# Optimization experiments

Hardware: AMD Instinct MI355X
Metric: run time of the kernel (lower is better)

The kernel has to match this reference:

```python
import jax, jax.numpy as jnp
import numpy as np

BATCH = 131072
INPUT_DIM = 256
HIDDEN = 128
DIM = 16
TRIL = DIM * (DIM + 1) // 2  # 136


def setup_inputs() -> dict:
    key = jax.random.key(0)
    k_x, k_w1, k_w2 = jax.random.split(key, 3)
    x = jax.random.normal(k_x, (BATCH, INPUT_DIM), dtype=jnp.float32)
    # Kaiming-ish init scaling so activations are well-conditioned
    W1 = jax.random.normal(k_w1, (INPUT_DIM, HIDDEN), dtype=jnp.float32) * (1.0 / np.sqrt(INPUT_DIM))
    b1 = jnp.zeros((HIDDEN,), dtype=jnp.float32)
    W2 = jax.random.normal(k_w2, (HIDDEN, TRIL), dtype=jnp.float32) * (1.0 / np.sqrt(HIDDEN))
    b2 = jnp.zeros((TRIL,), dtype=jnp.float32)
    return {"x": x, "W1": W1, "b1": b1, "W2": W2, "b2": b2}


def reference(x, W1, b1, W2, b2):
    # MLP: Linear -> ReLU -> Linear, producing tril entries of Cholesky factor
    h = jax.nn.relu(x @ W1 + b1)              # [B, 128]
    v = h @ W2 + b2                           # [B, 136]
    ti, tj = jnp.tril_indices(DIM)            # row-major tril order, matches torch.tril_indices
    L = jnp.zeros((x.shape[0], DIM, DIM), dtype=v.dtype).at[:, ti, tj].set(v)  # [B, D, D]
    rho = jnp.einsum('bik,bjk->bij', L, L)    # L @ L^T (real, so conj is no-op)
    trace = jnp.einsum('bii->b', rho)         # diagonal sum
    return rho / trace[:, None, None]
```

## Files before the change

### kernel.cpp

```cpp
#include <hip/hip_runtime.h>


typedef _Float16 h8 __attribute__((ext_vector_type(8)));
typedef float    f4 __attribute__((ext_vector_type(4)));
typedef int      i2 __attribute__((ext_vector_type(2)));

#define BATCH_N 131072
#define IN_DIM  256
#define HID     128
#define TRILN   136
#define BM      128
#define NT1     8
#define KS1     8
#define NT2     9
#define KS2     4
#define HSTR    136
#define LVSTR   160
#define PW1_N   (KS1*NT1*64*8)
#define PW2_N   (KS2*NT2*64*8)

__device__ __forceinline__ int rowoff(int i) {
    int g = i >> 2;
    return 4 * (g + 1) * (2 * g + (i & 3));
}

__global__ void pack_weights(const float* __restrict__ W1,
                             const float* __restrict__ W2,
                             _Float16* __restrict__ pw1,
                             _Float16* __restrict__ pw2) {
    int gid = blockIdx.x * blockDim.x + threadIdx.x;
    if (gid < PW1_N) {
        int j = gid & 7, l = (gid >> 3) & 63, f = gid >> 9;
        int ks = f >> 3, nt = f & 7;
        int k = ks * 32 + (l >> 4) * 8 + j;
        int n = nt * 16 + (l & 15);
        pw1[gid] = (_Float16)W1[k * HID + n];
    } else if (gid < PW1_N + PW2_N) {
        int g = gid - PW1_N;
        int j = g & 7, l = (g >> 3) & 63, f = g >> 9;
        int ks = f / NT2, nt = f - ks * NT2;
        int k = ks * 32 + (l >> 4) * 8 + j;
        int col = nt * 16 + (l & 15);
        pw2[g] = (col < TRILN) ? (_Float16)W2[k * TRILN + col] : (_Float16)0.0f;
    }
}

__device__ __forceinline__ h8 cvt_h8(f4 lo, f4 hi) {
    h8 r;
    r[0] = (_Float16)lo[0]; r[1] = (_Float16)lo[1];
    r[2] = (_Float16)lo[2]; r[3] = (_Float16)lo[3];
    r[4] = (_Float16)hi[0]; r[5] = (_Float16)hi[1];
    r[6] = (_Float16)hi[2]; r[7] = (_Float16)hi[3];
    return r;
}

__global__ __launch_bounds__(256, 4) void fused_mlp(
        const float* __restrict__ x, const float* __restrict__ b1,
        const float* __restrict__ b2, const _Float16* __restrict__ pw1,
        const _Float16* __restrict__ pw2, float* __restrict__ out) {
    __shared__ char smem_raw[BM * LVSTR * 2] __attribute__((aligned(16)));
    _Float16* hbuf = (_Float16*)smem_raw;
    _Float16* lv   = (_Float16*)smem_raw;

    const int tid  = threadIdx.x;
    const int w    = tid >> 6;
    const int lane = tid & 63;
    const int q    = lane >> 4;
    const int lm   = lane & 15;
    const int b0   = blockIdx.x * BM;

    f4 acc1[2][NT1];
    #pragma unroll
    for (int mt = 0; mt < 2; ++mt)
        #pragma unroll
        for (int nt = 0; nt < NT1; ++nt)
            acc1[mt][nt] = (f4){0.f, 0.f, 0.f, 0.f};

    const float* xr0 = x + (size_t)(b0 + w * 16 + lm) * IN_DIM + q * 8;
    const float* xr1 = xr0 + (size_t)64 * IN_DIM;

    f4 a0l = *(const f4*)xr0, a0h = *(const f4*)(xr0 + 4);
    f4 a1l = *(const f4*)xr1, a1h = *(const f4*)(xr1 + 4);

    #pragma unroll
    for (int ks = 0; ks < KS1; ++ks) {
        h8 bf[NT1];
        #pragma unroll
        for (int nt = 0; nt < NT1; ++nt)
            bf[nt] = *(const h8*)(pw1 + ((ks * NT1 + nt) * 64 + lane) * 8);
        h8 af0 = cvt_h8(a0l, a0h);
        h8 af1 = cvt_h8(a1l, a1h);
        if (ks + 1 < KS1) {
            const float* p0 = xr0 + (ks + 1) * 32;
            const float* p1 = xr1 + (ks + 1) * 32;
            a0l = *(const f4*)p0; a0h = *(const f4*)(p0 + 4);
            a1l = *(const f4*)p1; a1h = *(const f4*)(p1 + 4);
        }
        #pragma unroll
        for (int nt = 0; nt < NT1; ++nt) {
            acc1[0][nt] = __builtin_amdgcn_mfma_f32_16x16x32_f16(af0, bf[nt], acc1[0][nt], 0, 0, 0);
            acc1[1][nt] = __builtin_amdgcn_mfma_f32_16x16x32_f16(af1, bf[nt], acc1[1][nt], 0, 0, 0);
        }
    }

    {
        float b1v[NT1];
        #pragma unroll
        for (int nt = 0; nt < NT1; ++nt) b1v[nt] = b1[nt * 16 + lm];
        #pragma unroll
        for (int mt = 0; mt < 2; ++mt)
            #pragma unroll
            for (int nt = 0; nt < NT1; ++nt)
                #pragma unroll
                for (int r = 0; r < 4; ++r) {
                    float hv = acc1[mt][nt][r] + b1v[nt];
                    hv = fmaxf(hv, 0.f);
                    hbuf[(mt * 64 + w * 16 + q * 4 + r) * HSTR + nt * 16 + lm] = (_Float16)hv;
                }
    }

    f4 acc2[2][NT2];
    #pragma unroll
    for (int mt = 0; mt < 2; ++mt)
        #pragma unroll
        for (int nt = 0; nt < NT2; ++nt)
            acc2[mt][nt] = (f4){0.f, 0.f, 0.f, 0.f};

    #pragma unroll
    for (int ks = 0; ks < KS2; ++ks) {
        h8 ha0 = *(const h8*)(hbuf + (w * 16 + lm) * HSTR + ks * 32 + q * 8);
        h8 ha1 = *(const h8*)(hbuf + (64 + w * 16 + lm) * HSTR + ks * 32 + q * 8);
        #pragma unroll
        for (int nt = 0; nt < NT2; ++nt) {
            h8 bf = *(const h8*)(pw2 + ((ks * NT2 + nt) * 64 + lane) * 8);
            acc2[0][nt] = __builtin_amdgcn_mfma_f32_16x16x32_f16(ha0, bf, acc2[0][nt], 0, 0, 0);
            acc2[1][nt] = __builtin_amdgcn_mfma_f32_16x16x32_f16(ha1, bf, acc2[1][nt], 0, 0, 0);
        }
    }

    float b2v[NT2];
    #pragma unroll
    for (int nt = 0; nt < NT2; ++nt) {
        int col = nt * 16 + lm;
        b2v[nt] = (col < TRILN) ? b2[col] : 0.f;
    }

    float ps[2][4];
    #pragma unroll
    for (int mt = 0; mt < 2; ++mt)
        #pragma unroll
        for (int r = 0; r < 4; ++r) ps[mt][r] = 0.f;
    #pragma unroll
    for (int mt = 0; mt < 2; ++mt)
        #pragma unroll
        for (int nt = 0; nt < NT2; ++nt)
            #pragma unroll
            for (int r = 0; r < 4; ++r) {
                float v = acc2[mt][nt][r] + b2v[nt];
                ps[mt][r] += v * v;
            }

    float rinv[2][4];
    #pragma unroll
    for (int mt = 0; mt < 2; ++mt)
        #pragma unroll
        for (int r = 0; r < 4; ++r) {
            float s = ps[mt][r];
            s += __shfl_xor(s, 1);
            s += __shfl_xor(s, 2);
            s += __shfl_xor(s, 4);
            s += __shfl_xor(s, 8);
            rinv[mt][r] = 1.0f / s;
        }

    int voff[NT2];
    bool vok[NT2];
    #pragma unroll
    for (int nt = 0; nt < NT2; ++nt) {
        int c = nt * 16 + lm;
        vok[nt] = (c < TRILN);
        int cc = vok[nt] ? c : 0;
        int i = (int)((sqrtf(8.0f * (float)cc + 1.0f) - 1.0f) * 0.5f);
        int k = cc - (i * (i + 1)) / 2;
        voff[nt] = rowoff(i) + k;
    }

    __syncthreads();

    #pragma unroll
    for (int mt = 0; mt < 2; ++mt)
        #pragma unroll
        for (int r = 0; r < 4; ++r) {
            int base = (mt * 64 + w * 16 + q * 4 + r) * LVSTR;
            #pragma unroll
            for (int nt = 0; nt < NT2; ++nt)
                if (vok[nt])
                    lv[base + voff[nt]] = (_Float16)(acc2[mt][nt][r] + b2v[nt]);
        }

    int msk[4];
    {
        int n = lm - q * 8 + 1;
        #pragma unroll
        for (int p = 0; p < 4; ++p) {
            int c2 = n - 2 * p; c2 = c2 < 0 ? 0 : (c2 > 2 ? 2 : c2);
            msk[p] = (c2 == 2) ? ~0 : ((c2 == 1) ? 0xFFFF : 0);
        }
    }
    const int ro_lm = rowoff(lm);
    const f4 zero = (f4){0.f, 0.f, 0.f, 0.f};
    const int outcol = q * 64 + lm;

    #pragma unroll
    for (int mt = 0; mt < 2; ++mt)
        #pragma unroll
        for (int tq = 0; tq < 4; ++tq)
            #pragma unroll
            for (int r4 = 0; r4 < 4; ++r4) {
                int t = tq * 4 + r4;
                int row = mt * 64 + w * 16 + t;
                const _Float16* rp = lv + row * LVSTR + ro_lm + q * 8;
                i2 lo = *(const i2*)rp;
                i2 hi = *(const i2*)(rp + 4);
                h8 frag;
                ((i2*)&frag)[0] = (i2){lo.x & msk[0], lo.y & msk[1]};
                ((i2*)&frag)[1] = (i2){hi.x & msk[2], hi.y & msk[3]};
                f4 d = __builtin_amdgcn_mfma_f32_16x16x32_f16(frag, frag, zero, 0, 0, 0);
                float riv = __uint_as_float(
                    __builtin_amdgcn_readlane(__float_as_uint(rinv[mt][r4]), tq * 16));
                float* op = out + (size_t)(b0 + row) * 256 + outcol;
                #pragma unroll
                for (int sr = 0; sr < 4; ++sr)
                    op[sr * 16] = d[sr] * riv;
            }
}

extern "C" void kernel_launch(void* const* d_in, const int* in_sizes, int n_in,
                              void* d_out, int out_size, void* d_ws, size_t ws_size,
                              hipStream_t stream) {
    const float* x  = (const float*)d_in[0];
    const float* W1 = (const float*)d_in[1];
    const float* b1 = (const float*)d_in[2];
    const float* W2 = (const float*)d_in[3];
    const float* b2 = (const float*)d_in[4];
    float* out = (float*)d_out;

    _Float16* pw1 = (_Float16*)d_ws;
    _Float16* pw2 = pw1 + PW1_N;

    pack_weights<<<(PW1_N + PW2_N + 255) / 256, 256, 0, stream>>>(W1, W2, pw1, pw2);
    fused_mlp<<<BATCH_N / BM, 256, 0, stream>>>(x, b1, b2, pw1, pw2, out);
}
```

Before: 263.3 us.

## Process M-tiles sequentially per wave with private LDS regions and deeper x prefetch

Restructures the fused kernel so each wave handles its two 16-row M-tiles one after another instead of together. Each wave gets a private LDS region, so the block-wide __syncthreads is removed. The x loads for the second tile are prefetched during the first tile's epilogue, and the x prefetch depth goes from one k-step to four. This halves accumulator register pressure and lets memory loads overlap with compute, at the cost of less reuse of the W1/W2 fragments loaded per MFMA and twice the weight loads.

```diff
diff --git a/kernel.cpp b/kernel.cpp
--- a/kernel.cpp
+++ b/kernel.cpp
@@ -16,6 +16,7 @@
 #define KS2     4
 #define HSTR    136
 #define LVSTR   160
+#define MTREG   2560
 #define PW1_N   (KS1*NT1*64*8)
 #define PW2_N   (KS2*NT2*64*8)
 
@@ -54,13 +55,105 @@
     return r;
 }
 
+#define TAIL(MTBASE, MT)                                                       \
+  do {                                                                         \
+          \
+    _Pragma("unroll")                                                          \
+    for (int nt = 0; nt < NT1; ++nt) {                                         \
+      float b1v = b1[nt * 16 + lm];                                            \
+      _Pragma("unroll")                                                        \
+      for (int r = 0; r < 4; ++r) {                                            \
+        float hv = fmaxf(acc[nt][r] + b1v, 0.f);                               \
+        (MTBASE)[(q * 4 + r) * HSTR + nt * 16 + lm] = (_Float16)hv;            \
+      }                                                                        \
+    }                                                                          \
+                                                        \
+    f4 acc2[NT2];                                                              \
+    _Pragma("unroll")                                                          \
+    for (int nt = 0; nt < NT2; ++nt) acc2[nt] = (f4){0.f, 0.f, 0.f, 0.f};      \
+    _Pragma("unroll")                                                          \
+    for (int ks = 0; ks < KS2; ++ks) {                                         \
+      h8 ha = *(const h8*)((MTBASE) + lm * HSTR + ks * 32 + q * 8);            \
+      _Pragma("unroll")                                                        \
+      for (int nt = 0; nt < NT2; ++nt) {                                       \
+        h8 bf2 = *(const h8*)(pw2 + ((ks * NT2 + nt) * 64 + lane) * 8);        \
+        acc2[nt] = __builtin_amdgcn_mfma_f32_16x16x32_f16(ha, bf2, acc2[nt], 0, 0, 0); \
+      }                                                                        \
+    }                                                                          \
+    if ((MT) == 0) {                                                           \
+       \
+       \
+      _Pragma("unroll")                                                        \
+      for (int k = 0; k < 4; ++k) {                                            \
+        xp[2 * k]     = *(const f4*)(xr1 + k * 32);                            \
+        xp[2 * k + 1] = *(const f4*)(xr1 + k * 32 + 4);                        \
+      }                                                                        \
+      __builtin_amdgcn_sched_barrier(0);                                       \
+    }                                                                          \
+                                            \
+    float b2v[NT2];                                                            \
+    int voff[NT2]; bool vok[NT2];                                              \
+    _Pragma("unroll")                                                          \
+    for (int nt = 0; nt < NT2; ++nt) {                                         \
+      int c = nt * 16 + lm;                                                    \
+      vok[nt] = (c < TRILN);                                                   \
+      int cc = vok[nt] ? c : 0;                                                \
+      int i = (int)((sqrtf(8.0f * (float)cc + 1.0f) - 1.0f) * 0.5f);           \
+      int k = cc - (i * (i + 1)) / 2;                                          \
+      voff[nt] = rowoff(i) + k;                                                \
+      b2v[nt] = vok[nt] ? b2[c] : 0.f;                                         \
+    }                                                                          \
+       \
+    float rinv[4];                                                             \
+    _Pragma("unroll")                                                          \
+    for (int r = 0; r < 4; ++r) {                                              \
+      float s = 0.f;                                                           \
+      _Pragma("unroll")                                                        \
+      for (int nt = 0; nt < NT2; ++nt) {                                       \
+        float v = acc2[nt][r] + b2v[nt];                                       \
+        s += v * v;                                                            \
+      }                                                                        \
+      s += __shfl_xor(s, 1); s += __shfl_xor(s, 2);                            \
+      s += __shfl_xor(s, 4); s += __shfl_xor(s, 8);                            \
+      rinv[r] = 1.0f / s;                                                      \
+    }                                                                          \
+     \
+     \
+    _Pragma("unroll")                                                          \
+    for (int r = 0; r < 4; ++r) {                                              \
+      int base = (q * 4 + r) * LVSTR;                                          \
+      _Pragma("unroll")                                                        \
+      for (int nt = 0; nt < NT2; ++nt)                                         \
+        if (vok[nt])                                                           \
+          (MTBASE)[base + voff[nt]] = (_Float16)(acc2[nt][r] + b2v[nt]);       \
+    }                                                                          \
+                  \
+    _Pragma("unroll")                                                          \
+    for (int tq = 0; tq < 4; ++tq)                                             \
+      _Pragma("unroll")                                                        \
+      for (int r4 = 0; r4 < 4; ++r4) {                                         \
+        int t = tq * 4 + r4;                                                   \
+        const _Float16* rp = (MTBASE) + t * LVSTR + ro_lm + q * 8;             \
+        i2 lo = *(const i2*)rp;                                                \
+        i2 hi = *(const i2*)(rp + 4);                                          \
+        h8 frag;                                                               \
+        ((i2*)&frag)[0] = (i2){lo.x & msk[0], lo.y & msk[1]};                  \
+        ((i2*)&frag)[1] = (i2){hi.x & msk[2], hi.y & msk[3]};                  \
+        f4 d = __builtin_amdgcn_mfma_f32_16x16x32_f16(frag, frag, zero, 0, 0, 0); \
+        float riv = __uint_as_float(                                           \
+            __builtin_amdgcn_readlane(__float_as_uint(rinv[r4]), tq * 16));    \
+        float* op = out + (size_t)(b0 + (MT) * 64 + w * 16 + t) * 256 + outcol;\
+        _Pragma("unroll")                                                      \
+        for (int sr = 0; sr < 4; ++sr)                                         \
+          op[sr * 16] = d[sr] * riv;           \
+      }                                                                        \
+  } while (0)
+
 __global__ __launch_bounds__(256, 4) void fused_mlp(
         const float* __restrict__ x, const float* __restrict__ b1,
         const float* __restrict__ b2, const _Float16* __restrict__ pw1,
         const _Float16* __restrict__ pw2, float* __restrict__ out) {
-    __shared__ char smem_raw[BM * LVSTR * 2] __attribute__((aligned(16)));
-    _Float16* hbuf = (_Float16*)smem_raw;
-    _Float16* lv   = (_Float16*)smem_raw;
+    __shared__ _Float16 smem[4 * 2 * MTREG] __attribute__((aligned(16)));
 
     const int tid  = threadIdx.x;
     const int w    = tid >> 6;
@@ -69,18 +162,61 @@
     const int lm   = lane & 15;
     const int b0   = blockIdx.x * BM;
 
-    f4 acc1[2][NT1];
-    #pragma unroll
-    for (int mt = 0; mt < 2; ++mt)
-        #pragma unroll
-        for (int nt = 0; nt < NT1; ++nt)
-            acc1[mt][nt] = (f4){0.f, 0.f, 0.f, 0.f};
+    _Float16* mt0base = smem + w * (2 * MTREG);
+    _Float16* mt1base = mt0base + MTREG;
+
+    const int ro_lm  = rowoff(lm);
+    const int outcol = q * 64 + lm;
+    const f4 zero = (f4){0.f, 0.f, 0.f, 0.f};
+
+    int msk[4];
+    {
+        int n = lm - q * 8 + 1;
+        #pragma unroll
+        for (int p = 0; p < 4; ++p) {
+            int c2 = n - 2 * p; c2 = c2 < 0 ? 0 : (c2 > 2 ? 2 : c2);
+            msk[p] = (c2 == 2) ? ~0 : ((c2 == 1) ? 0xFFFF : 0);
+        }
+    }
 
     const float* xr0 = x + (size_t)(b0 + w * 16 + lm) * IN_DIM + q * 8;
     const float* xr1 = xr0 + (size_t)64 * IN_DIM;
 
-    f4 a0l = *(const f4*)xr0, a0h = *(const f4*)(xr0 + 4);
-    f4 a1l = *(const f4*)xr1, a1h = *(const f4*)(xr1 + 4);
+    f4 xp[8];
+
+    f4 acc[NT1];
+    #pragma unroll
+    for (int nt = 0; nt < NT1; ++nt) acc[nt] = (f4){0.f, 0.f, 0.f, 0.f};
+
+    {
+        f4 xw[8];
+        #pragma unroll
+        for (int k = 0; k < 4; ++k) {
+            xw[2 * k]     = *(const f4*)(xr0 + k * 32);
+            xw[2 * k + 1] = *(const f4*)(xr0 + k * 32 + 4);
+        }
+
+        #pragma unroll
+        for (int ks = 0; ks < KS1; ++ks) {
+            h8 bf[NT1];
+            #pragma unroll
+            for (int nt = 0; nt < NT1; ++nt)
+                bf[nt] = *(const h8*)(pw1 + ((ks * NT1 + nt) * 64 + lane) * 8);
+            h8 af = cvt_h8(xw[(ks & 3) * 2], xw[(ks & 3) * 2 + 1]);
+            if (ks + 4 < KS1) {
+                xw[(ks & 3) * 2]     = *(const f4*)(xr0 + (ks + 4) * 32);
+                xw[(ks & 3) * 2 + 1] = *(const f4*)(xr0 + (ks + 4) * 32 + 4);
+            }
+            #pragma unroll
+            for (int nt = 0; nt < NT1; ++nt)
+                acc[nt] = __builtin_amdgcn_mfma_f32_16x16x32_f16(af, bf[nt], acc[nt], 0, 0, 0);
+        }
+    }
+
+    TAIL(mt0base, 0);
+
+    #pragma unroll
+    for (int nt = 0; nt < NT1; ++nt) acc[nt] = (f4){0.f, 0.f, 0.f, 0.f};
 
     #pragma unroll
     for (int ks = 0; ks < KS1; ++ks) {
@@ -88,151 +224,17 @@
         #pragma unroll
         for (int nt = 0; nt < NT1; ++nt)
             bf[nt] = *(const h8*)(pw1 + ((ks * NT1 + nt) * 64 + lane) * 8);
-        h8 af0 = cvt_h8(a0l, a0h);
-        h8 af1 = cvt_h8(a1l, a1h);
-        if (ks + 1 < KS1) {
-            const float* p0 = xr0 + (ks + 1) * 32;
-            const float* p1 = xr1 + (ks + 1) * 32;
-            a0l = *(const f4*)p0; a0h = *(const f4*)(p0 + 4);
-            a1l = *(const f4*)p1; a1h = *(const f4*)(p1 + 4);
-        }
-        #pragma unroll
-        for (int nt = 0; nt < NT1; ++nt) {
-            acc1[0][nt] = __builtin_amdgcn_mfma_f32_16x16x32_f16(af0, bf[nt], acc1[0][nt], 0, 0, 0);
-            acc1[1][nt] = __builtin_amdgcn_mfma_f32_16x16x32_f16(af1, bf[nt], acc1[1][nt], 0, 0, 0);
-        }
-    }
-
-    {
-        float b1v[NT1];
-        #pragma unroll
-        for (int nt = 0; nt < NT1; ++nt) b1v[nt] = b1[nt * 16 + lm];
-        #pragma unroll
-        for (int mt = 0; mt < 2; ++mt)
-            #pragma unroll
-            for (int nt = 0; nt < NT1; ++nt)
-                #pragma unroll
-                for (int r = 0; r < 4; ++r) {
-                    float hv = acc1[mt][nt][r] + b1v[nt];
-                    hv = fmaxf(hv, 0.f);
-                    hbuf[(mt * 64 + w * 16 + q * 4 + r) * HSTR + nt * 16 + lm] = (_Float16)hv;
-                }
-    }
-
-    f4 acc2[2][NT2];
-    #pragma unroll
-    for (int mt = 0; mt < 2; ++mt)
-        #pragma unroll
-        for (int nt = 0; nt < NT2; ++nt)
-            acc2[mt][nt] = (f4){0.f, 0.f, 0.f, 0.f};
-
-    #pragma unroll
-    for (int ks = 0; ks < KS2; ++ks) {
-        h8 ha0 = *(const h8*)(hbuf + (w * 16 + lm) * HSTR + ks * 32 + q * 8);
-        h8 ha1 = *(const h8*)(hbuf + (64 + w * 16 + lm) * HSTR + ks * 32 + q * 8);
-        #pragma unroll
-        for (int nt = 0; nt < NT2; ++nt) {
-            h8 bf = *(const h8*)(pw2 + ((ks * NT2 + nt) * 64 + lane) * 8);
-            acc2[0][nt] = __builtin_amdgcn_mfma_f32_16x16x32_f16(ha0, bf, acc2[0][nt], 0, 0, 0);
-            acc2[1][nt] = __builtin_amdgcn_mfma_f32_16x16x32_f16(ha1, bf, acc2[1][nt], 0, 0, 0);
-        }
-    }
-
-    float b2v[NT2];
-    #pragma unroll
-    for (int nt = 0; nt < NT2; ++nt) {
-        int col = nt * 16 + lm;
-        b2v[nt] = (col < TRILN) ? b2[col] : 0.f;
-    }
-
-    float ps[2][4];
-    #pragma unroll
-    for (int mt = 0; mt < 2; ++mt)
-        #pragma unroll
-        for (int r = 0; r < 4; ++r) ps[mt][r] = 0.f;
-    #pragma unroll
-    for (int mt = 0; mt < 2; ++mt)
-        #pragma unroll
-        for (int nt = 0; nt < NT2; ++nt)
-            #pragma unroll
-            for (int r = 0; r < 4; ++r) {
-                float v = acc2[mt][nt][r] + b2v[nt];
-                ps[mt][r] += v * v;
-            }
-
-    float rinv[2][4];
-    #pragma unroll
-    for (int mt = 0; mt < 2; ++mt)
-        #pragma unroll
-        for (int r = 0; r < 4; ++r) {
-            float s = ps[mt][r];
-            s += __shfl_xor(s, 1);
-            s += __shfl_xor(s, 2);
-            s += __shfl_xor(s, 4);
-            s += __shfl_xor(s, 8);
-            rinv[mt][r] = 1.0f / s;
-        }
-
-    int voff[NT2];
-    bool vok[NT2];
-    #pragma unroll
-    for (int nt = 0; nt < NT2; ++nt) {
-        int c = nt * 16 + lm;
-        vok[nt] = (c < TRILN);
-        int cc = vok[nt] ? c : 0;
-        int i = (int)((sqrtf(8.0f * (float)cc + 1.0f) - 1.0f) * 0.5f);
-        int k = cc - (i * (i + 1)) / 2;
-        voff[nt] = rowoff(i) + k;
-    }
-
-    __syncthreads();
-
-    #pragma unroll
-    for (int mt = 0; mt < 2; ++mt)
-        #pragma unroll
-        for (int r = 0; r < 4; ++r) {
-            int base = (mt * 64 + w * 16 + q * 4 + r) * LVSTR;
-            #pragma unroll
-            for (int nt = 0; nt < NT2; ++nt)
-                if (vok[nt])
-                    lv[base + voff[nt]] = (_Float16)(acc2[mt][nt][r] + b2v[nt]);
-        }
-
-    int msk[4];
-    {
-        int n = lm - q * 8 + 1;
-        #pragma unroll
-        for (int p = 0; p < 4; ++p) {
-            int c2 = n - 2 * p; c2 = c2 < 0 ? 0 : (c2 > 2 ? 2 : c2);
-            msk[p] = (c2 == 2) ? ~0 : ((c2 == 1) ? 0xFFFF : 0);
-        }
-    }
-    const int ro_lm = rowoff(lm);
-    const f4 zero = (f4){0.f, 0.f, 0.f, 0.f};
-    const int outcol = q * 64 + lm;
-
-    #pragma unroll
-    for (int mt = 0; mt < 2; ++mt)
-        #pragma unroll
-        for (int tq = 0; tq < 4; ++tq)
-            #pragma unroll
-            for (int r4 = 0; r4 < 4; ++r4) {
-                int t = tq * 4 + r4;
-                int row = mt * 64 + w * 16 + t;
-                const _Float16* rp = lv + row * LVSTR + ro_lm + q * 8;
-                i2 lo = *(const i2*)rp;
-                i2 hi = *(const i2*)(rp + 4);
-                h8 frag;
-                ((i2*)&frag)[0] = (i2){lo.x & msk[0], lo.y & msk[1]};
-                ((i2*)&frag)[1] = (i2){hi.x & msk[2], hi.y & msk[3]};
-                f4 d = __builtin_amdgcn_mfma_f32_16x16x32_f16(frag, frag, zero, 0, 0, 0);
-                float riv = __uint_as_float(
-                    __builtin_amdgcn_readlane(__float_as_uint(rinv[mt][r4]), tq * 16));
-                float* op = out + (size_t)(b0 + row) * 256 + outcol;
-                #pragma unroll
-                for (int sr = 0; sr < 4; ++sr)
-                    op[sr * 16] = d[sr] * riv;
-            }
+        h8 af = cvt_h8(xp[(ks & 3) * 2], xp[(ks & 3) * 2 + 1]);
+        if (ks + 4 < KS1) {
+            xp[(ks & 3) * 2]     = *(const f4*)(xr1 + (ks + 4) * 32);
+            xp[(ks & 3) * 2 + 1] = *(const f4*)(xr1 + (ks + 4) * 32 + 4);
+        }
+        #pragma unroll
+        for (int nt = 0; nt < NT1; ++nt)
+            acc[nt] = __builtin_amdgcn_mfma_f32_16x16x32_f16(af, bf[nt], acc[nt], 0, 0, 0);
+    }
+
+    TAIL(mt1base, 1);
 }
 
 extern "C" void kernel_launch(void* const* d_in, const int* in_sizes, int n_in,
```

Result: slower. 395.1 us (+50.1%).

## Process row tiles per warp sequentially with private LDS and vectorized stores

Applied to the files above, without the earlier changes.

Each warp now handles its two 16-row tiles one after the other, using a private LDS region for the hidden activations and the tril scatter. This removes the block-wide barrier, halves shared memory use and cuts live accumulator registers, which should allow more resident waves. The x prefetch is deepened to four k-steps, and output writes use the symmetry of L·Lᵀ to emit contiguous float4 stores instead of strided scalar stores. In exchange there is less MFMA overlap between the two tiles within a wave, and correctness relies on ordering of LDS accesses within a single wave.

```diff
diff --git a/kernel.cpp b/kernel.cpp
--- a/kernel.cpp
+++ b/kernel.cpp
@@ -16,6 +16,7 @@
 #define KS2     4
 #define HSTR    136
 #define LVSTR   160
+#define MTREG   2560
 #define PW1_N   (KS1*NT1*64*8)
 #define PW2_N   (KS2*NT2*64*8)
 
@@ -58,9 +59,7 @@
         const float* __restrict__ x, const float* __restrict__ b1,
         const float* __restrict__ b2, const _Float16* __restrict__ pw1,
         const _Float16* __restrict__ pw2, float* __restrict__ out) {
-    __shared__ char smem_raw[BM * LVSTR * 2] __attribute__((aligned(16)));
-    _Float16* hbuf = (_Float16*)smem_raw;
-    _Float16* lv   = (_Float16*)smem_raw;
+    __shared__ _Float16 smem[4 * MTREG] __attribute__((aligned(16)));
 
     const int tid  = threadIdx.x;
     const int w    = tid >> 6;
@@ -69,134 +68,10 @@
     const int lm   = lane & 15;
     const int b0   = blockIdx.x * BM;
 
-    f4 acc1[2][NT1];
-    #pragma unroll
-    for (int mt = 0; mt < 2; ++mt)
-        #pragma unroll
-        for (int nt = 0; nt < NT1; ++nt)
-            acc1[mt][nt] = (f4){0.f, 0.f, 0.f, 0.f};
-
-    const float* xr0 = x + (size_t)(b0 + w * 16 + lm) * IN_DIM + q * 8;
-    const float* xr1 = xr0 + (size_t)64 * IN_DIM;
-
-    f4 a0l = *(const f4*)xr0, a0h = *(const f4*)(xr0 + 4);
-    f4 a1l = *(const f4*)xr1, a1h = *(const f4*)(xr1 + 4);
-
-    #pragma unroll
-    for (int ks = 0; ks < KS1; ++ks) {
-        h8 bf[NT1];
-        #pragma unroll
-        for (int nt = 0; nt < NT1; ++nt)
-            bf[nt] = *(const h8*)(pw1 + ((ks * NT1 + nt) * 64 + lane) * 8);
-        h8 af0 = cvt_h8(a0l, a0h);
-        h8 af1 = cvt_h8(a1l, a1h);
-        if (ks + 1 < KS1) {
-            const float* p0 = xr0 + (ks + 1) * 32;
-            const float* p1 = xr1 + (ks + 1) * 32;
-            a0l = *(const f4*)p0; a0h = *(const f4*)(p0 + 4);
-            a1l = *(const f4*)p1; a1h = *(const f4*)(p1 + 4);
-        }
-        #pragma unroll
-        for (int nt = 0; nt < NT1; ++nt) {
-            acc1[0][nt] = __builtin_amdgcn_mfma_f32_16x16x32_f16(af0, bf[nt], acc1[0][nt], 0, 0, 0);
-            acc1[1][nt] = __builtin_amdgcn_mfma_f32_16x16x32_f16(af1, bf[nt], acc1[1][nt], 0, 0, 0);
-        }
-    }
-
-    {
-        float b1v[NT1];
-        #pragma unroll
-        for (int nt = 0; nt < NT1; ++nt) b1v[nt] = b1[nt * 16 + lm];
-        #pragma unroll
-        for (int mt = 0; mt < 2; ++mt)
-            #pragma unroll
-            for (int nt = 0; nt < NT1; ++nt)
-                #pragma unroll
-                for (int r = 0; r < 4; ++r) {
-                    float hv = acc1[mt][nt][r] + b1v[nt];
-                    hv = fmaxf(hv, 0.f);
-                    hbuf[(mt * 64 + w * 16 + q * 4 + r) * HSTR + nt * 16 + lm] = (_Float16)hv;
-                }
-    }
-
-    f4 acc2[2][NT2];
-    #pragma unroll
-    for (int mt = 0; mt < 2; ++mt)
-        #pragma unroll
-        for (int nt = 0; nt < NT2; ++nt)
-            acc2[mt][nt] = (f4){0.f, 0.f, 0.f, 0.f};
-
-    #pragma unroll
-    for (int ks = 0; ks < KS2; ++ks) {
-        h8 ha0 = *(const h8*)(hbuf + (w * 16 + lm) * HSTR + ks * 32 + q * 8);
-        h8 ha1 = *(const h8*)(hbuf + (64 + w * 16 + lm) * HSTR + ks * 32 + q * 8);
-        #pragma unroll
-        for (int nt = 0; nt < NT2; ++nt) {
-            h8 bf = *(const h8*)(pw2 + ((ks * NT2 + nt) * 64 + lane) * 8);
-            acc2[0][nt] = __builtin_amdgcn_mfma_f32_16x16x32_f16(ha0, bf, acc2[0][nt], 0, 0, 0);
-            acc2[1][nt] = __builtin_amdgcn_mfma_f32_16x16x32_f16(ha1, bf, acc2[1][nt], 0, 0, 0);
-        }
-    }
-
-    float b2v[NT2];
-    #pragma unroll
-    for (int nt = 0; nt < NT2; ++nt) {
-        int col = nt * 16 + lm;
-        b2v[nt] = (col < TRILN) ? b2[col] : 0.f;
-    }
-
-    float ps[2][4];
-    #pragma unroll
-    for (int mt = 0; mt < 2; ++mt)
-        #pragma unroll
-        for (int r = 0; r < 4; ++r) ps[mt][r] = 0.f;
-    #pragma unroll
-    for (int mt = 0; mt < 2; ++mt)
-        #pragma unroll
-        for (int nt = 0; nt < NT2; ++nt)
-            #pragma unroll
-            for (int r = 0; r < 4; ++r) {
-                float v = acc2[mt][nt][r] + b2v[nt];
-                ps[mt][r] += v * v;
-            }
-
-    float rinv[2][4];
-    #pragma unroll
-    for (int mt = 0; mt < 2; ++mt)
-        #pragma unroll
-        for (int r = 0; r < 4; ++r) {
-            float s = ps[mt][r];
-            s += __shfl_xor(s, 1);
-            s += __shfl_xor(s, 2);
-            s += __shfl_xor(s, 4);
-            s += __shfl_xor(s, 8);
-            rinv[mt][r] = 1.0f / s;
-        }
-
-    int voff[NT2];
-    bool vok[NT2];
-    #pragma unroll
-    for (int nt = 0; nt < NT2; ++nt) {
-        int c = nt * 16 + lm;
-        vok[nt] = (c < TRILN);
-        int cc = vok[nt] ? c : 0;
-        int i = (int)((sqrtf(8.0f * (float)cc + 1.0f) - 1.0f) * 0.5f);
-        int k = cc - (i * (i + 1)) / 2;
-        voff[nt] = rowoff(i) + k;
-    }
-
-    __syncthreads();
-
-    #pragma unroll
-    for (int mt = 0; mt < 2; ++mt)
-        #pragma unroll
-        for (int r = 0; r < 4; ++r) {
-            int base = (mt * 64 + w * 16 + q * 4 + r) * LVSTR;
-            #pragma unroll
-            for (int nt = 0; nt < NT2; ++nt)
-                if (vok[nt])
-                    lv[base + voff[nt]] = (_Float16)(acc2[mt][nt][r] + b2v[nt]);
-        }
+    _Float16* reg0 = smem + w * MTREG;
+
+    const int ro_lm = rowoff(lm);
+    const f4 zero = (f4){0.f, 0.f, 0.f, 0.f};
 
     int msk[4];
     {
@@ -207,19 +82,106 @@
             msk[p] = (c2 == 2) ? ~0 : ((c2 == 1) ? 0xFFFF : 0);
         }
     }
-    const int ro_lm = rowoff(lm);
-    const f4 zero = (f4){0.f, 0.f, 0.f, 0.f};
-    const int outcol = q * 64 + lm;
+
+    const float* xrw = x + (size_t)(b0 + w * 16 + lm) * IN_DIM + q * 8;
 
     #pragma unroll
-    for (int mt = 0; mt < 2; ++mt)
+    for (int mt = 0; mt < 2; ++mt) {
+        const float* xr = xrw + (size_t)(mt * 64) * IN_DIM;
+
+        f4 acc[NT1];
+        #pragma unroll
+        for (int nt = 0; nt < NT1; ++nt) acc[nt] = (f4){0.f, 0.f, 0.f, 0.f};
+
+        {
+            f4 xw[8];
+            #pragma unroll
+            for (int k = 0; k < 4; ++k) {
+                xw[2 * k]     = *(const f4*)(xr + k * 32);
+                xw[2 * k + 1] = *(const f4*)(xr + k * 32 + 4);
+            }
+            #pragma unroll
+            for (int ks = 0; ks < KS1; ++ks) {
+                h8 bf[NT1];
+                #pragma unroll
+                for (int nt = 0; nt < NT1; ++nt)
+                    bf[nt] = *(const h8*)(pw1 + ((ks * NT1 + nt) * 64 + lane) * 8);
+                h8 af = cvt_h8(xw[(ks & 3) * 2], xw[(ks & 3) * 2 + 1]);
+                if (ks + 4 < KS1) {
+                    xw[(ks & 3) * 2]     = *(const f4*)(xr + (ks + 4) * 32);
+                    xw[(ks & 3) * 2 + 1] = *(const f4*)(xr + (ks + 4) * 32 + 4);
+                }
+                #pragma unroll
+                for (int nt = 0; nt < NT1; ++nt)
+                    acc[nt] = __builtin_amdgcn_mfma_f32_16x16x32_f16(af, bf[nt], acc[nt], 0, 0, 0);
+            }
+        }
+
+        #pragma unroll
+        for (int nt = 0; nt < NT1; ++nt) {
+            float b1v = b1[nt * 16 + lm];
+            #pragma unroll
+            for (int r = 0; r < 4; ++r) {
+                float hv = fmaxf(acc[nt][r] + b1v, 0.f);
+                reg0[(q * 4 + r) * HSTR + nt * 16 + lm] = (_Float16)hv;
+            }
+        }
+
+        f4 acc2[NT2];
+        #pragma unroll
+        for (int nt = 0; nt < NT2; ++nt) acc2[nt] = (f4){0.f, 0.f, 0.f, 0.f};
+        #pragma unroll
+        for (int ks = 0; ks < KS2; ++ks) {
+            h8 ha = *(const h8*)(reg0 + lm * HSTR + ks * 32 + q * 8);
+            #pragma unroll
+            for (int nt = 0; nt < NT2; ++nt) {
+                h8 bf2 = *(const h8*)(pw2 + ((ks * NT2 + nt) * 64 + lane) * 8);
+                acc2[nt] = __builtin_amdgcn_mfma_f32_16x16x32_f16(ha, bf2, acc2[nt], 0, 0, 0);
+            }
+        }
+
+        float b2v[NT2];
+        int voff[NT2]; bool vok[NT2];
+        #pragma unroll
+        for (int nt = 0; nt < NT2; ++nt) {
+            int c = nt * 16 + lm;
+            vok[nt] = (c < TRILN);
+            int cc = vok[nt] ? c : 0;
+            int i = (int)((sqrtf(8.0f * (float)cc + 1.0f) - 1.0f) * 0.5f);
+            int k = cc - (i * (i + 1)) / 2;
+            voff[nt] = rowoff(i) + k;
+            b2v[nt] = vok[nt] ? b2[c] : 0.f;
+        }
+
+        float rinv[4];
+        #pragma unroll
+        for (int r = 0; r < 4; ++r) {
+            float s = 0.f;
+            #pragma unroll
+            for (int nt = 0; nt < NT2; ++nt) {
+                float v = acc2[nt][r] + b2v[nt];
+                s += v * v;
+            }
+            s += __shfl_xor(s, 1); s += __shfl_xor(s, 2);
+            s += __shfl_xor(s, 4); s += __shfl_xor(s, 8);
+            rinv[r] = 1.0f / s;
+        }
+
+        #pragma unroll
+        for (int r = 0; r < 4; ++r) {
+            int base = (q * 4 + r) * LVSTR;
+            #pragma unroll
+            for (int nt = 0; nt < NT2; ++nt)
+                if (vok[nt])
+                    reg0[base + voff[nt]] = (_Float16)(acc2[nt][r] + b2v[nt]);
+        }
+
         #pragma unroll
         for (int tq = 0; tq < 4; ++tq)
             #pragma unroll
             for (int r4 = 0; r4 < 4; ++r4) {
                 int t = tq * 4 + r4;
-                int row = mt * 64 + w * 16 + t;
-                const _Float16* rp = lv + row * LVSTR + ro_lm + q * 8;
+                const _Float16* rp = reg0 + t * LVSTR + ro_lm + q * 8;
                 i2 lo = *(const i2*)rp;
                 i2 hi = *(const i2*)(rp + 4);
                 h8 frag;
@@ -227,12 +189,11 @@
                 ((i2*)&frag)[1] = (i2){hi.x & msk[2], hi.y & msk[3]};
                 f4 d = __builtin_amdgcn_mfma_f32_16x16x32_f16(frag, frag, zero, 0, 0, 0);
                 float riv = __uint_as_float(
-                    __builtin_amdgcn_readlane(__float_as_uint(rinv[mt][r4]), tq * 16));
-                float* op = out + (size_t)(b0 + row) * 256 + outcol;
-                #pragma unroll
-                for (int sr = 0; sr < 4; ++sr)
-                    op[sr * 16] = d[sr] * riv;
-            }
+                    __builtin_amdgcn_readlane(__float_as_uint(rinv[r4]), tq * 16));
+                f4 dv = d * riv;
+                *(f4*)(out + (size_t)(b0 + mt * 64 + w * 16 + t) * 256 + lm * 16 + q * 4) = dv;
+            }
+    }
 }
 
 extern "C" void kernel_launch(void* const* d_in, const int* in_sizes, int n_in,
```

New measurement: 379.1 us. 1.44x slower.

## Give each wave private LDS regions, drop block barrier, vectorize output stores

Applied to the files above, without the earlier changes.

The single shared LDS buffer is split into per-wave regions for the hidden activations and the L factor, which removes the block-wide __syncthreads before the L scatter. The output write is changed from four strided scalar stores per lane to one 16-byte vector store, relying on the symmetry of rho to transpose the index mapping. sched_barrier fences are added between phases to constrain compiler scheduling. Total LDS size is unchanged; the fences may limit overlap of loads with MFMA work.

```diff
diff --git a/kernel.cpp b/kernel.cpp
--- a/kernel.cpp
+++ b/kernel.cpp
@@ -16,8 +16,11 @@
 #define KS2     4
 #define HSTR    136
 #define LVSTR   160
+#define MTREG   2560
 #define PW1_N   (KS1*NT1*64*8)
 #define PW2_N   (KS2*NT2*64*8)
+
+#define FENCE() __builtin_amdgcn_sched_barrier(0)
 
 __device__ __forceinline__ int rowoff(int i) {
     int g = i >> 2;
@@ -58,9 +61,7 @@
         const float* __restrict__ x, const float* __restrict__ b1,
         const float* __restrict__ b2, const _Float16* __restrict__ pw1,
         const _Float16* __restrict__ pw2, float* __restrict__ out) {
-    __shared__ char smem_raw[BM * LVSTR * 2] __attribute__((aligned(16)));
-    _Float16* hbuf = (_Float16*)smem_raw;
-    _Float16* lv   = (_Float16*)smem_raw;
+    __shared__ _Float16 smem[4 * 2 * MTREG] __attribute__((aligned(16)));
 
     const int tid  = threadIdx.x;
     const int w    = tid >> 6;
@@ -68,6 +69,23 @@
     const int q    = lane >> 4;
     const int lm   = lane & 15;
     const int b0   = blockIdx.x * BM;
+
+    _Float16* reg[2];
+    reg[0] = smem + w * (2 * MTREG);
+    reg[1] = reg[0] + MTREG;
+
+    const int ro_lm = rowoff(lm);
+    const f4 zero = (f4){0.f, 0.f, 0.f, 0.f};
+
+    int msk[4];
+    {
+        int n = lm - q * 8 + 1;
+        #pragma unroll
+        for (int p = 0; p < 4; ++p) {
+            int c2 = n - 2 * p; c2 = c2 < 0 ? 0 : (c2 > 2 ? 2 : c2);
+            msk[p] = (c2 == 2) ? ~0 : ((c2 == 1) ? 0xFFFF : 0);
+        }
+    }
 
     f4 acc1[2][NT1];
     #pragma unroll
@@ -103,6 +121,8 @@
         }
     }
 
+    FENCE();
+
     {
         float b1v[NT1];
         #pragma unroll
@@ -113,11 +133,12 @@
             for (int nt = 0; nt < NT1; ++nt)
                 #pragma unroll
                 for (int r = 0; r < 4; ++r) {
-                    float hv = acc1[mt][nt][r] + b1v[nt];
-                    hv = fmaxf(hv, 0.f);
-                    hbuf[(mt * 64 + w * 16 + q * 4 + r) * HSTR + nt * 16 + lm] = (_Float16)hv;
+                    float hv = fmaxf(acc1[mt][nt][r] + b1v[nt], 0.f);
+                    reg[mt][(q * 4 + r) * HSTR + nt * 16 + lm] = (_Float16)hv;
                 }
     }
+
+    FENCE();
 
     f4 acc2[2][NT2];
     #pragma unroll
@@ -128,53 +149,20 @@
 
     #pragma unroll
     for (int ks = 0; ks < KS2; ++ks) {
-        h8 ha0 = *(const h8*)(hbuf + (w * 16 + lm) * HSTR + ks * 32 + q * 8);
-        h8 ha1 = *(const h8*)(hbuf + (64 + w * 16 + lm) * HSTR + ks * 32 + q * 8);
+        h8 ha0 = *(const h8*)(reg[0] + lm * HSTR + ks * 32 + q * 8);
+        h8 ha1 = *(const h8*)(reg[1] + lm * HSTR + ks * 32 + q * 8);
         #pragma unroll
         for (int nt = 0; nt < NT2; ++nt) {
-            h8 bf = *(const h8*)(pw2 + ((ks * NT2 + nt) * 64 + lane) * 8);
-            acc2[0][nt] = __builtin_amdgcn_mfma_f32_16x16x32_f16(ha0, bf, acc2[0][nt], 0, 0, 0);
-            acc2[1][nt] = __builtin_amdgcn_mfma_f32_16x16x32_f16(ha1, bf, acc2[1][nt], 0, 0, 0);
-        }
-    }
+            h8 bf2 = *(const h8*)(pw2 + ((ks * NT2 + nt) * 64 + lane) * 8);
+            acc2[0][nt] = __builtin_amdgcn_mfma_f32_16x16x32_f16(ha0, bf2, acc2[0][nt], 0, 0, 0);
+            acc2[1][nt] = __builtin_amdgcn_mfma_f32_16x16x32_f16(ha1, bf2, acc2[1][nt], 0, 0, 0);
+        }
+    }
+
+    FENCE();
 
     float b2v[NT2];
-    #pragma unroll
-    for (int nt = 0; nt < NT2; ++nt) {
-        int col = nt * 16 + lm;
-        b2v[nt] = (col < TRILN) ? b2[col] : 0.f;
-    }
-
-    float ps[2][4];
-    #pragma unroll
-    for (int mt = 0; mt < 2; ++mt)
-        #pragma unroll
-        for (int r = 0; r < 4; ++r) ps[mt][r] = 0.f;
-    #pragma unroll
-    for (int mt = 0; mt < 2; ++mt)
-        #pragma unroll
-        for (int nt = 0; nt < NT2; ++nt)
-            #pragma unroll
-            for (int r = 0; r < 4; ++r) {
-                float v = acc2[mt][nt][r] + b2v[nt];
-                ps[mt][r] += v * v;
-            }
-
-    float rinv[2][4];
-    #pragma unroll
-    for (int mt = 0; mt < 2; ++mt)
-        #pragma unroll
-        for (int r = 0; r < 4; ++r) {
-            float s = ps[mt][r];
-            s += __shfl_xor(s, 1);
-            s += __shfl_xor(s, 2);
-            s += __shfl_xor(s, 4);
-            s += __shfl_xor(s, 8);
-            rinv[mt][r] = 1.0f / s;
-        }
-
-    int voff[NT2];
-    bool vok[NT2];
+    int voff[NT2]; bool vok[NT2];
     #pragma unroll
     for (int nt = 0; nt < NT2; ++nt) {
         int c = nt * 16 + lm;
@@ -183,33 +171,37 @@
         int i = (int)((sqrtf(8.0f * (float)cc + 1.0f) - 1.0f) * 0.5f);
         int k = cc - (i * (i + 1)) / 2;
         voff[nt] = rowoff(i) + k;
-    }
-
-    __syncthreads();
-
+        b2v[nt] = vok[nt] ? b2[c] : 0.f;
+    }
+
+    float rinv[2][4];
     #pragma unroll
     for (int mt = 0; mt < 2; ++mt)
         #pragma unroll
         for (int r = 0; r < 4; ++r) {
-            int base = (mt * 64 + w * 16 + q * 4 + r) * LVSTR;
+            float s = 0.f;
+            #pragma unroll
+            for (int nt = 0; nt < NT2; ++nt) {
+                float v = acc2[mt][nt][r] + b2v[nt];
+                s += v * v;
+            }
+            s += __shfl_xor(s, 1); s += __shfl_xor(s, 2);
+            s += __shfl_xor(s, 4); s += __shfl_xor(s, 8);
+            rinv[mt][r] = 1.0f / s;
+        }
+
+    #pragma unroll
+    for (int mt = 0; mt < 2; ++mt)
+        #pragma unroll
+        for (int r = 0; r < 4; ++r) {
+            int base = (q * 4 + r) * LVSTR;
             #pragma unroll
             for (int nt = 0; nt < NT2; ++nt)
                 if (vok[nt])
-                    lv[base + voff[nt]] = (_Float16)(acc2[mt][nt][r] + b2v[nt]);
-        }
-
-    int msk[4];
-    {
-        int n = lm - q * 8 + 1;
-        #pragma unroll
-        for (int p = 0; p < 4; ++p) {
-            int c2 = n - 2 * p; c2 = c2 < 0 ? 0 : (c2 > 2 ? 2 : c2);
-            msk[p] = (c2 == 2) ? ~0 : ((c2 == 1) ? 0xFFFF : 0);
-        }
-    }
-    const int ro_lm = rowoff(lm);
-    const f4 zero = (f4){0.f, 0.f, 0.f, 0.f};
-    const int outcol = q * 64 + lm;
+                    reg[mt][base + voff[nt]] = (_Float16)(acc2[mt][nt][r] + b2v[nt]);
+        }
+
+    FENCE();
 
     #pragma unroll
     for (int mt = 0; mt < 2; ++mt)
@@ -218,8 +210,7 @@
             #pragma unroll
             for (int r4 = 0; r4 < 4; ++r4) {
                 int t = tq * 4 + r4;
-                int row = mt * 64 + w * 16 + t;
-                const _Float16* rp = lv + row * LVSTR + ro_lm + q * 8;
+                const _Float16* rp = reg[mt] + t * LVSTR + ro_lm + q * 8;
                 i2 lo = *(const i2*)rp;
                 i2 hi = *(const i2*)(rp + 4);
                 h8 frag;
@@ -228,10 +219,8 @@
                 f4 d = __builtin_amdgcn_mfma_f32_16x16x32_f16(frag, frag, zero, 0, 0, 0);
                 float riv = __uint_as_float(
                     __builtin_amdgcn_readlane(__float_as_uint(rinv[mt][r4]), tq * 16));
-                float* op = out + (size_t)(b0 + row) * 256 + outcol;
-                #pragma unroll
-                for (int sr = 0; sr < 4; ++sr)
-                    op[sr * 16] = d[sr] * riv;
+                f4 dv = d * riv;
+                *(f4*)(out + (size_t)(b0 + mt * 64 + w * 16 + t) * 256 + lm * 16 + q * 4) = dv;
             }
 }
 
```

Result: faster. 254.5 us (-3.3%).
